# Kernel optimization log

Hardware: AMD Instinct MI355X
Metric: run time of the kernel (lower is better)

Reference implementation:

```python
import jax, jax.numpy as jnp
import numpy as np

N, E = 50000, 500000
F_IN, F_OUT, H = 128, 16, 8  # in_features, out_features, n_head


def setup_inputs() -> dict:
    key = jax.random.key(0)
    k1, k2, k3, k4, k5, k6 = jax.random.split(key, 6)
    x = jax.random.normal(k1, (N, F_IN), dtype=jnp.float32)
    # xavier_normal with gain 1.414 (as in the torch init)
    w_std = 1.414 * np.sqrt(2.0 / (F_IN + F_OUT * H))
    weight = jax.random.normal(k2, (F_IN, F_OUT * H), dtype=jnp.float32) * w_std
    b_std = 1.414 * np.sqrt(2.0 / (F_OUT + H))
    bias = jax.random.normal(k3, (1, F_OUT, H), dtype=jnp.float32) * b_std
    a_std = 1.414 * np.sqrt(2.0 / (F_OUT + H))
    a2 = jax.random.normal(k4, (F_OUT, H), dtype=jnp.float32) * a_std
    edge_index = jax.random.randint(k5, (2, E), 0, N, dtype=jnp.int64)
    adj_vals = jax.random.uniform(k6, (E,), dtype=jnp.float32)
    return {"x": x, "edge_index": edge_index, "adj_vals": adj_vals,
            "weight": weight, "bias": bias, "a2": a2}


def _spmm(rows, cols, vals, X, n):
    # sparse (n,n) @ dense (n,d): gather source rows, scale, scatter-add to dest rows
    return jax.ops.segment_sum(vals[:, None] * X[cols], rows, num_segments=n)


def reference(x, edge_index, adj_vals, weight, bias, a2):
    n = x.shape[0]
    rows, cols = edge_index[0], edge_index[1]
    # support0: (N, F_OUT, H) -- torch .view(N, out_features, n_head)
    support0 = (x @ weight).reshape(n, F_OUT, H)
    mask = jnp.ones((n, 1, H), dtype=x.dtype)
    support = jnp.concatenate([support0, mask], axis=1)  # (N, F_OUT+1, H)
    # per-node, per-head attention scalar (softplus-like via sqrt)
    attn2 = jnp.einsum('aij,ij->aj', support[:, :-1, :], a2)  # (N, H)
    attn2 = attn2 + jnp.sqrt(attn2 * attn2 + 1.0)
    # post_attn_order = 1 iteration
    attn_support = (support * attn2[:, None, :]).reshape(n, (F_OUT + 1) * H)
    # pre_attn_order = 1 SpMM propagation (no APPNP)
    attn_support = _spmm(rows, cols, adj_vals, attn_support, n)
    support = attn_support.reshape(n, F_OUT + 1, H)
    # self-normalize by the propagated mask column
    output = support[:, :-1, :] / (support[:, -1:, :] + 1e-9)
    output = output + bias  # (N, F_OUT, H)
    return output.reshape(n, F_OUT * H)
```

## Files before the change

### kernel.cpp

```cpp
#include <hip/hip_runtime.h>
#include <hip/hip_bf16.h>


#define F 128
#define FP 136
#define NH 8
#define SCAN_ELEMS 1024
#define GN 16
#define XS 136
#define ZS2 128
#define HE 4

typedef __attribute__((ext_vector_type(8))) short bf16x8;
typedef __attribute__((ext_vector_type(4))) float f32x4;

static __device__ __forceinline__ unsigned short f2bf(float f) {
    __hip_bfloat16 h = __float2bfloat16(f);
    return *(unsigned short*)&h;
}
static __device__ __forceinline__ float bf_lo(unsigned int u) { return __uint_as_float(u << 16); }
static __device__ __forceinline__ float bf_hi(unsigned int u) { return __uint_as_float(u & 0xFFFF0000u); }

__global__ __launch_bounds__(256)
void k_prep_w(const float* __restrict__ w, unsigned short* __restrict__ wt,
              int* __restrict__ cnt, int ncnt, int* __restrict__ flagsum)
{
    int idx = blockIdx.x * 256 + threadIdx.x;
    int col = idx >> 7;
    int k   = idx & 127;
    wt[col * 128 + k] = f2bf(w[k * F + col]);
    if (idx < 64) flagsum[idx] = 0;
    for (int i = idx; i < ncnt; i += 64 * 256) cnt[i] = 0;
}

__global__ __launch_bounds__(128)
void k_gemm_hist(const float* __restrict__ x, const unsigned short* __restrict__ wt,
                 const float* __restrict__ a2, unsigned short* __restrict__ zm,
                 unsigned short* __restrict__ zk, int n,
                 const int* __restrict__ rows, int* __restrict__ cnt,
                 int* __restrict__ rank, int E, int G1, int G2)
{
    __shared__ __align__(16) unsigned short xls[GN * XS];
    __shared__ float part[2 * GN * 8];
    __shared__ float sarr[GN * 8];

    const int bid = blockIdx.x;
    const int t   = threadIdx.x;

    int gemm_id;
    {
        const int quota4 = G2 * 4;
        if (bid < quota4) {
            int q = bid >> 2, r = bid & 3;
            if (r == 3) {
                int base = (q * 128 + t) * HE;
                if (base < E) {
                    if (base + HE <= E) {
                        int4 r4 = *(const int4*)(rows + base);
                        int k0 = atomicAdd(&cnt[r4.x], 1);
                        int k1 = atomicAdd(&cnt[r4.y], 1);
                        int k2 = atomicAdd(&cnt[r4.z], 1);
                        int k3 = atomicAdd(&cnt[r4.w], 1);
                        *(int4*)(rank + base) = make_int4(k0, k1, k2, k3);
                    } else {
                        for (int e = base; e < E; ++e) rank[e] = atomicAdd(&cnt[rows[e]], 1);
                    }
                }
                return;
            }
            gemm_id = 3 * q + r;
        } else {
            gemm_id = bid - G2;
        }
    }
    if (gemm_id >= G1) return;

    const int l  = t & 63;
    const int w  = t >> 6;
    const int lm = l & 15;
    const int lq = l >> 4;
    const int n0 = gemm_id * GN;

    #pragma unroll
    for (int i = 0; i < 4; ++i) {
        int idx  = i * 128 + t;
        int node = idx >> 5;
        int k0   = (idx & 31) * 4;
        int gn   = n0 + node;
        float4 v = (gn < n) ? *(const float4*)(x + (long)gn * F + k0)
                            : make_float4(0.f, 0.f, 0.f, 0.f);
        ushort4 h;
        h.x = f2bf(v.x); h.y = f2bf(v.y); h.z = f2bf(v.z); h.w = f2bf(v.w);
        *(ushort4*)(&xls[node * XS + k0]) = h;
    }
    __syncthreads();

    const int wc = w * 64;
    f32x4 acc[4];
    #pragma unroll
    for (int cf = 0; cf < 4; ++cf) acc[cf] = (f32x4){0.f, 0.f, 0.f, 0.f};

    #pragma unroll
    for (int ks = 0; ks < 4; ++ks) {
        const int koff = ks * 32 + lq * 8;
        bf16x8 ah = *(const bf16x8*)(&xls[lm * XS + koff]);
        #pragma unroll
        for (int cf = 0; cf < 4; ++cf) {
            bf16x8 bh = *(const bf16x8*)(wt + (wc + cf * 16 + lm) * 128 + koff);
            acc[cf] = __builtin_amdgcn_mfma_f32_16x16x32_bf16(ah, bh, acc[cf], 0, 0, 0);
        }
    }

    float a2v[4];
    #pragma unroll
    for (int cf = 0; cf < 4; ++cf) a2v[cf] = a2[wc + cf * 16 + lm];
    const int j = l & 7;

    #pragma unroll
    for (int r = 0; r < 4; ++r) {
        float pl = 0.f;
        #pragma unroll
        for (int cf = 0; cf < 4; ++cf) pl = fmaf(acc[cf][r], a2v[cf], pl);
        pl += __shfl_xor(pl, 8, 64);
        if ((l & 8) == 0) {
            int node = lq * 4 + r;
            part[(w * GN + node) * 8 + j] = pl;
        }
    }
    __syncthreads();

    {
        int node = t >> 3;
        int jj   = t & 7;
        float ts = part[(0 * GN + node) * 8 + jj] + part[(1 * GN + node) * 8 + jj];
        float s = ts + sqrtf(ts * ts + 1.0f);
        sarr[node * 8 + jj] = s;
        int gn = n0 + node;
        if (gn < n) zk[(long)gn * NH + jj] = f2bf(s);
    }
    __syncthreads();

    #pragma unroll
    for (int r = 0; r < 4; ++r) {
        int node = lq * 4 + r;
        float sv = sarr[node * 8 + j];
        #pragma unroll
        for (int cf = 0; cf < 4; ++cf) {
            int c = wc + cf * 16 + lm;
            xls[node * ZS2 + c] = f2bf(acc[cf][r] * sv);
        }
    }
    __syncthreads();

    {
        int rows_here = n - n0; if (rows_here > GN) rows_here = GN;
        int nvec = rows_here * 16;
        const uint4* srcv = (const uint4*)xls;
        uint4* dstv = (uint4*)(zm + (size_t)n0 * F);
        #pragma unroll
        for (int i = 0; i < 2; ++i) {
            int idx = i * 128 + t;
            if (idx < nvec) dstv[idx] = srcv[idx];
        }
    }
}

__global__ __launch_bounds__(256)
void k_scan_one(const int* __restrict__ cnt, int* __restrict__ flagsum,
                int* __restrict__ start, int n, int E)
{
    const int b = blockIdx.x;
    const int t = threadIdx.x;
    const int lane = t & 63;
    const int wv = t >> 6;
    const int base = b * SCAN_ELEMS + t * 4;

    int v[4];
    int sum4 = 0;
    #pragma unroll
    for (int k = 0; k < 4; ++k) {
        int i = base + k;
        v[k] = (i < n) ? cnt[i] : 0;
        sum4 += v[k];
    }

    int incl = sum4;
    #pragma unroll
    for (int off = 1; off < 64; off <<= 1) {
        int u = __shfl_up(incl, off, 64);
        if (lane >= off) incl += u;
    }

    __shared__ int waveSums[4];
    __shared__ int boffs_sh;
    if (lane == 63) waveSums[wv] = incl;
    __syncthreads();
    if (t == 0) {
        int r = 0;
        #pragma unroll
        for (int w2 = 0; w2 < 4; ++w2) { int tmp = waveSums[w2]; waveSums[w2] = r; r += tmp; }
        atomicExch(&flagsum[b], r + 1);
    }

    if (t < 64) {
        int acc = 0;
        for (int i = lane; i < b; i += 64) {
            int f;
            while ((f = atomicAdd(&flagsum[i], 0)) == 0) { }
            acc += f - 1;
        }
        #pragma unroll
        for (int off = 32; off >= 1; off >>= 1) acc += __shfl_down(acc, off, 64);
        if (t == 0) boffs_sh = acc;
    }
    __syncthreads();

    int run = boffs_sh + waveSums[wv] + (incl - sum4);
    #pragma unroll
    for (int k = 0; k < 4; ++k) {
        int i = base + k;
        if (i < n) start[i] = run;
        run += v[k];
        if (i == n - 1) start[n] = E;
    }
}

__global__ __launch_bounds__(256)
void k_scatter(const int* __restrict__ rows, const int* __restrict__ cols,
               const float* __restrict__ vals, const int* __restrict__ start,
               const int* __restrict__ rank, int2* __restrict__ ce, int E)
{
    int base = (blockIdx.x * 256 + threadIdx.x) * 2;
    if (base >= E) return;
    if (base + 2 <= E) {
        int2   r2 = *(const int2*)(rows + base);
        int2   c2 = *(const int2*)(cols + base);
        float2 v2 = *(const float2*)(vals + base);
        int2   k2 = *(const int2*)(rank + base);
        ce[start[r2.x] + k2.x] = make_int2(c2.x, __float_as_int(v2.x));
        ce[start[r2.y] + k2.y] = make_int2(c2.y, __float_as_int(v2.y));
    } else {
        ce[start[rows[base]] + rank[base]] = make_int2(cols[base], __float_as_int(vals[base]));
    }
}

__global__ __launch_bounds__(256)
void k_spmm_pull(const int* __restrict__ start, const int2* __restrict__ ce,
                 const unsigned short* __restrict__ zm, const unsigned short* __restrict__ zk,
                 const float* __restrict__ bias, float* __restrict__ out, int n)
{
    const int grp  = (blockIdx.x * blockDim.x + threadIdx.x) >> 4;
    const int lane = threadIdx.x & 63;
    const int c16  = lane & 15;
    if (grp >= n) return;

    const int mq  = c16 & 3;
    const int s0  = start[grp];
    const int end = start[grp + 1];

    float az[8];
    #pragma unroll
    for (int k = 0; k < 8; ++k) az[k] = 0.f;
    float am0 = 0.f, am1 = 0.f;

    for (int e = s0; e < end; e += 4) {
        int e1 = (e + 1 < end) ? e + 1 : end - 1;
        int e2 = (e + 2 < end) ? e + 2 : end - 1;
        int e3 = (e + 3 < end) ? e + 3 : end - 1;
        int2 p0 = ce[e];
        int2 p1 = ce[e1];
        int2 p2 = ce[e2];
        int2 p3 = ce[e3];
        float v0 = __int_as_float(p0.y);
        float v1 = (e + 1 < end) ? __int_as_float(p1.y) : 0.f;
        float v2 = (e + 2 < end) ? __int_as_float(p2.y) : 0.f;
        float v3 = (e + 3 < end) ? __int_as_float(p3.y) : 0.f;
        uint4 d0 = ((const uint4*)zm)[(long)p0.x * 16 + c16];
        uint4 d1 = ((const uint4*)zm)[(long)p1.x * 16 + c16];
        uint4 d2 = ((const uint4*)zm)[(long)p2.x * 16 + c16];
        uint4 d3 = ((const uint4*)zm)[(long)p3.x * 16 + c16];
        unsigned int m0 = *(const unsigned int*)(zk + (long)p0.x * NH + 2 * mq);
        unsigned int m1 = *(const unsigned int*)(zk + (long)p1.x * NH + 2 * mq);
        unsigned int m2 = *(const unsigned int*)(zk + (long)p2.x * NH + 2 * mq);
        unsigned int m3 = *(const unsigned int*)(zk + (long)p3.x * NH + 2 * mq);

        az[0] = fmaf(v0, bf_lo(d0.x), az[0]);  az[1] = fmaf(v0, bf_hi(d0.x), az[1]);
        az[2] = fmaf(v0, bf_lo(d0.y), az[2]);  az[3] = fmaf(v0, bf_hi(d0.y), az[3]);
        az[4] = fmaf(v0, bf_lo(d0.z), az[4]);  az[5] = fmaf(v0, bf_hi(d0.z), az[5]);
        az[6] = fmaf(v0, bf_lo(d0.w), az[6]);  az[7] = fmaf(v0, bf_hi(d0.w), az[7]);
        am0   = fmaf(v0, bf_lo(m0), am0);      am1   = fmaf(v0, bf_hi(m0), am1);

        az[0] = fmaf(v1, bf_lo(d1.x), az[0]);  az[1] = fmaf(v1, bf_hi(d1.x), az[1]);
        az[2] = fmaf(v1, bf_lo(d1.y), az[2]);  az[3] = fmaf(v1, bf_hi(d1.y), az[3]);
        az[4] = fmaf(v1, bf_lo(d1.z), az[4]);  az[5] = fmaf(v1, bf_hi(d1.z), az[5]);
        az[6] = fmaf(v1, bf_lo(d1.w), az[6]);  az[7] = fmaf(v1, bf_hi(d1.w), az[7]);
        am0   = fmaf(v1, bf_lo(m1), am0);      am1   = fmaf(v1, bf_hi(m1), am1);

        az[0] = fmaf(v2, bf_lo(d2.x), az[0]);  az[1] = fmaf(v2, bf_hi(d2.x), az[1]);
        az[2] = fmaf(v2, bf_lo(d2.y), az[2]);  az[3] = fmaf(v2, bf_hi(d2.y), az[3]);
        az[4] = fmaf(v2, bf_lo(d2.z), az[4]);  az[5] = fmaf(v2, bf_hi(d2.z), az[5]);
        az[6] = fmaf(v2, bf_lo(d2.w), az[6]);  az[7] = fmaf(v2, bf_hi(d2.w), az[7]);
        am0   = fmaf(v2, bf_lo(m2), am0);      am1   = fmaf(v2, bf_hi(m2), am1);

        az[0] = fmaf(v3, bf_lo(d3.x), az[0]);  az[1] = fmaf(v3, bf_hi(d3.x), az[1]);
        az[2] = fmaf(v3, bf_lo(d3.y), az[2]);  az[3] = fmaf(v3, bf_hi(d3.y), az[3]);
        az[4] = fmaf(v3, bf_lo(d3.z), az[4]);  az[5] = fmaf(v3, bf_hi(d3.z), az[5]);
        az[6] = fmaf(v3, bf_lo(d3.w), az[6]);  az[7] = fmaf(v3, bf_hi(d3.w), az[7]);
        am0   = fmaf(v3, bf_lo(m3), am0);      am1   = fmaf(v3, bf_hi(m3), am1);
    }

    const int gb = lane & 48;
    float den[8];
    den[0] = __shfl(am0, gb + 0, 64);  den[1] = __shfl(am1, gb + 0, 64);
    den[2] = __shfl(am0, gb + 1, 64);  den[3] = __shfl(am1, gb + 1, 64);
    den[4] = __shfl(am0, gb + 2, 64);  den[5] = __shfl(am1, gb + 2, 64);
    den[6] = __shfl(am0, gb + 3, 64);  den[7] = __shfl(am1, gb + 3, 64);

    const float* bp = bias + 8 * c16;
    float4 b0v = *(const float4*)(bp);
    float4 b1v = *(const float4*)(bp + 4);
    float4 o0, o1;
    o0.x = az[0] / (den[0] + 1e-9f) + b0v.x;
    o0.y = az[1] / (den[1] + 1e-9f) + b0v.y;
    o0.z = az[2] / (den[2] + 1e-9f) + b0v.z;
    o0.w = az[3] / (den[3] + 1e-9f) + b0v.w;
    o1.x = az[4] / (den[4] + 1e-9f) + b1v.x;
    o1.y = az[5] / (den[5] + 1e-9f) + b1v.y;
    o1.z = az[6] / (den[6] + 1e-9f) + b1v.z;
    o1.w = az[7] / (den[7] + 1e-9f) + b1v.w;
    float* op = out + (long)grp * F + 8 * c16;
    *(float4*)(op)     = o0;
    *(float4*)(op + 4) = o1;
}

extern "C" void kernel_launch(void* const* d_in, const int* in_sizes, int n_in,
                              void* d_out, int out_size, void* d_ws, size_t ws_size,
                              hipStream_t stream)
{
    const float* x    = (const float*)d_in[0];
    const int*   ei   = (const int*)d_in[1];
    const float* vals = (const float*)d_in[2];
    const float* w    = (const float*)d_in[3];
    const float* bias = (const float*)d_in[4];
    const float* a2   = (const float*)d_in[5];
    float* out = (float*)d_out;

    const int N = in_sizes[0] / F;
    const int E = in_sizes[2];
    const int* rows = ei;
    const int* cols = ei + E;

    const int nblk = (N + SCAN_ELEMS - 1) / SCAN_ELEMS;
    const int G1 = (N + GN - 1) / GN;
    const int G2 = (E + 128 * HE - 1) / (128 * HE);

    char* p = (char*)d_ws;
    unsigned short* zm = (unsigned short*)p;  p += (size_t)N * F * sizeof(unsigned short);
    unsigned short* zk = (unsigned short*)p;  p += (((size_t)N * NH * sizeof(unsigned short) + 255) & ~255ull);
    unsigned short* wt = (unsigned short*)p;  p += 128 * 128 * sizeof(unsigned short);
    int*   cnt      = (int*)p;    p += ((size_t)N + 64) * sizeof(int);
    int*   start    = (int*)p;    p += ((size_t)N + 64) * sizeof(int);
    int*   flagsum  = (int*)p;    p += 64 * sizeof(int);
    int*   rank     = (int*)p;    p += (size_t)E * sizeof(int);
    int2*  ce       = (int2*)p;

    k_prep_w<<<dim3(64), dim3(256), 0, stream>>>(w, wt, cnt, N, flagsum);

    k_gemm_hist<<<dim3(G1 + G2), dim3(128), 0, stream>>>(x, wt, a2, zm, zk, N,
                                                         rows, cnt, rank, E, G1, G2);

    k_scan_one<<<dim3(nblk), dim3(256), 0, stream>>>(cnt, flagsum, start, N, E);

    k_scatter<<<dim3((E / 2 + 255) / 256), dim3(256), 0, stream>>>(rows, cols, vals, start, rank, ce, E);

    dim3 b5(256), g5(((size_t)N * 16 + 255) / 256);
    k_spmm_pull<<<g5, b5, 0, stream>>>(start, ce, zm, zk, bias, out, N);
}
```

Baseline: 77.71 us.

## Shrink GEMM/histogram blocks to one wavefront and drop shared-memory reductions

Each fused GEMM/histogram block now runs as a single 64-lane wavefront. One wave computes all 128 output columns for 16 nodes with 8 MFMA accumulators, so the cross-wave partial sums in shared memory and the __syncthreads barriers go away, and the attention scalar is computed in registers after a shuffle. Histogram blocks process 8 edges per thread, which keeps the edge count per block at 512. The cost is higher register use per wave, fewer threads per block, and reliance on single-wave LDS ordering with no barriers.

```diff
diff --git a/kernel.cpp b/kernel.cpp
--- a/kernel.cpp
+++ b/kernel.cpp
@@ -3,13 +3,11 @@
 
 
 #define F 128
-#define FP 136
 #define NH 8
 #define SCAN_ELEMS 1024
 #define GN 16
 #define XS 136
-#define ZS2 128
-#define HE 4
+#define HE 8
 
 typedef __attribute__((ext_vector_type(8))) short bf16x8;
 typedef __attribute__((ext_vector_type(4))) float f32x4;
@@ -33,7 +31,7 @@
     for (int i = idx; i < ncnt; i += 64 * 256) cnt[i] = 0;
 }
 
-__global__ __launch_bounds__(128)
+__global__ __launch_bounds__(64)
 void k_gemm_hist(const float* __restrict__ x, const unsigned short* __restrict__ wt,
                  const float* __restrict__ a2, unsigned short* __restrict__ zm,
                  unsigned short* __restrict__ zk, int n,
@@ -41,8 +39,6 @@
                  int* __restrict__ rank, int E, int G1, int G2)
 {
     __shared__ __align__(16) unsigned short xls[GN * XS];
-    __shared__ float part[2 * GN * 8];
-    __shared__ float sarr[GN * 8];
 
     const int bid = blockIdx.x;
     const int t   = threadIdx.x;
@@ -53,15 +49,21 @@
         if (bid < quota4) {
             int q = bid >> 2, r = bid & 3;
             if (r == 3) {
-                int base = (q * 128 + t) * HE;
+                int base = (q * 64 + t) * HE;
                 if (base < E) {
                     if (base + HE <= E) {
-                        int4 r4 = *(const int4*)(rows + base);
-                        int k0 = atomicAdd(&cnt[r4.x], 1);
-                        int k1 = atomicAdd(&cnt[r4.y], 1);
-                        int k2 = atomicAdd(&cnt[r4.z], 1);
-                        int k3 = atomicAdd(&cnt[r4.w], 1);
-                        *(int4*)(rank + base) = make_int4(k0, k1, k2, k3);
+                        int4 ra = *(const int4*)(rows + base);
+                        int4 rb = *(const int4*)(rows + base + 4);
+                        int k0 = atomicAdd(&cnt[ra.x], 1);
+                        int k1 = atomicAdd(&cnt[ra.y], 1);
+                        int k2 = atomicAdd(&cnt[ra.z], 1);
+                        int k3 = atomicAdd(&cnt[ra.w], 1);
+                        int k4 = atomicAdd(&cnt[rb.x], 1);
+                        int k5 = atomicAdd(&cnt[rb.y], 1);
+                        int k6 = atomicAdd(&cnt[rb.z], 1);
+                        int k7 = atomicAdd(&cnt[rb.w], 1);
+                        *(int4*)(rank + base)     = make_int4(k0, k1, k2, k3);
+                        *(int4*)(rank + base + 4) = make_int4(k4, k5, k6, k7);
                     } else {
                         for (int e = base; e < E; ++e) rank[e] = atomicAdd(&cnt[rows[e]], 1);
                     }
@@ -75,15 +77,13 @@
     }
     if (gemm_id >= G1) return;
 
-    const int l  = t & 63;
-    const int w  = t >> 6;
-    const int lm = l & 15;
-    const int lq = l >> 4;
+    const int lm = t & 15;
+    const int lq = t >> 4;
     const int n0 = gemm_id * GN;
 
     #pragma unroll
-    for (int i = 0; i < 4; ++i) {
-        int idx  = i * 128 + t;
+    for (int i = 0; i < 8; ++i) {
+        int idx  = i * 64 + t;
         int node = idx >> 5;
         int k0   = (idx & 31) * 4;
         int gn   = n0 + node;
@@ -93,64 +93,51 @@
         h.x = f2bf(v.x); h.y = f2bf(v.y); h.z = f2bf(v.z); h.w = f2bf(v.w);
         *(ushort4*)(&xls[node * XS + k0]) = h;
     }
-    __syncthreads();
-
-    const int wc = w * 64;
-    f32x4 acc[4];
-    #pragma unroll
-    for (int cf = 0; cf < 4; ++cf) acc[cf] = (f32x4){0.f, 0.f, 0.f, 0.f};
+
+    f32x4 acc[8];
+    #pragma unroll
+    for (int cf = 0; cf < 8; ++cf) acc[cf] = (f32x4){0.f, 0.f, 0.f, 0.f};
 
     #pragma unroll
     for (int ks = 0; ks < 4; ++ks) {
         const int koff = ks * 32 + lq * 8;
         bf16x8 ah = *(const bf16x8*)(&xls[lm * XS + koff]);
         #pragma unroll
-        for (int cf = 0; cf < 4; ++cf) {
-            bf16x8 bh = *(const bf16x8*)(wt + (wc + cf * 16 + lm) * 128 + koff);
+        for (int cf = 0; cf < 8; ++cf) {
+            bf16x8 bh = *(const bf16x8*)(wt + (cf * 16 + lm) * 128 + koff);
             acc[cf] = __builtin_amdgcn_mfma_f32_16x16x32_bf16(ah, bh, acc[cf], 0, 0, 0);
         }
     }
 
-    float a2v[4];
-    #pragma unroll
-    for (int cf = 0; cf < 4; ++cf) a2v[cf] = a2[wc + cf * 16 + lm];
-    const int j = l & 7;
-
+    float a2v[8];
+    #pragma unroll
+    for (int cf = 0; cf < 8; ++cf) a2v[cf] = a2[cf * 16 + lm];
+
+    float s4[4];
     #pragma unroll
     for (int r = 0; r < 4; ++r) {
         float pl = 0.f;
         #pragma unroll
-        for (int cf = 0; cf < 4; ++cf) pl = fmaf(acc[cf][r], a2v[cf], pl);
+        for (int cf = 0; cf < 8; ++cf) pl = fmaf(acc[cf][r], a2v[cf], pl);
         pl += __shfl_xor(pl, 8, 64);
-        if ((l & 8) == 0) {
-            int node = lq * 4 + r;
-            part[(w * GN + node) * 8 + j] = pl;
-        }
-    }
-    __syncthreads();
-
-    {
-        int node = t >> 3;
-        int jj   = t & 7;
-        float ts = part[(0 * GN + node) * 8 + jj] + part[(1 * GN + node) * 8 + jj];
-        float s = ts + sqrtf(ts * ts + 1.0f);
-        sarr[node * 8 + jj] = s;
-        int gn = n0 + node;
-        if (gn < n) zk[(long)gn * NH + jj] = f2bf(s);
-    }
-    __syncthreads();
+        s4[r] = pl + sqrtf(pl * pl + 1.0f);
+    }
+
+    if (lm < NH) {
+        #pragma unroll
+        for (int r = 0; r < 4; ++r) {
+            int gn = n0 + lq * 4 + r;
+            if (gn < n) zk[(long)gn * NH + lm] = f2bf(s4[r]);
+        }
+    }
 
     #pragma unroll
     for (int r = 0; r < 4; ++r) {
         int node = lq * 4 + r;
-        float sv = sarr[node * 8 + j];
-        #pragma unroll
-        for (int cf = 0; cf < 4; ++cf) {
-            int c = wc + cf * 16 + lm;
-            xls[node * ZS2 + c] = f2bf(acc[cf][r] * sv);
-        }
-    }
-    __syncthreads();
+        #pragma unroll
+        for (int cf = 0; cf < 8; ++cf)
+            xls[node * 128 + cf * 16 + lm] = f2bf(acc[cf][r] * s4[r]);
+    }
 
     {
         int rows_here = n - n0; if (rows_here > GN) rows_here = GN;
@@ -158,8 +145,8 @@
         const uint4* srcv = (const uint4*)xls;
         uint4* dstv = (uint4*)(zm + (size_t)n0 * F);
         #pragma unroll
-        for (int i = 0; i < 2; ++i) {
-            int idx = i * 128 + t;
+        for (int i = 0; i < 4; ++i) {
+            int idx = i * 64 + t;
             if (idx < nvec) dstv[idx] = srcv[idx];
         }
     }
@@ -352,7 +339,7 @@
 
     const int nblk = (N + SCAN_ELEMS - 1) / SCAN_ELEMS;
     const int G1 = (N + GN - 1) / GN;
-    const int G2 = (E + 128 * HE - 1) / (128 * HE);
+    const int G2 = (E + 64 * HE - 1) / (64 * HE);
 
     char* p = (char*)d_ws;
     unsigned short* zm = (unsigned short*)p;  p += (size_t)N * F * sizeof(unsigned short);
@@ -366,8 +353,8 @@
 
     k_prep_w<<<dim3(64), dim3(256), 0, stream>>>(w, wt, cnt, N, flagsum);
 
-    k_gemm_hist<<<dim3(G1 + G2), dim3(128), 0, stream>>>(x, wt, a2, zm, zk, N,
-                                                         rows, cnt, rank, E, G1, G2);
+    k_gemm_hist<<<dim3(G1 + G2), dim3(64), 0, stream>>>(x, wt, a2, zm, zk, N,
+                                                        rows, cnt, rank, E, G1, G2);
 
     k_scan_one<<<dim3(nblk), dim3(256), 0, stream>>>(cnt, flagsum, start, N, E);
 
```

After: 79.01 us. No clear change (+1.7%).
